# Kernel tuning notes

Measured on AMD Instinct MI355X. Metric: run time of the kernel, lower is better.

Reference implementation:

```python
import jax, jax.numpy as jnp
import numpy as np

DIM = 1024
NUM_HEADS = 16
HEAD_DIM = DIM // NUM_HEADS
SCALE = HEAD_DIM ** -0.5


def setup_inputs() -> dict:
    key = jax.random.key(0)
    k1, k2, k3 = jax.random.split(key, 3)
    x = jax.random.normal(k1, (2, 2048, DIM), dtype=jnp.float32)
    # nn.Linear weights: stored as [out, in]; y = x @ W.T
    w_qkv = jax.random.normal(k2, (3 * DIM, DIM), dtype=jnp.float32) * (DIM ** -0.5)
    w_proj = jax.random.normal(k3, (DIM, DIM), dtype=jnp.float32) * (DIM ** -0.5)
    return {"x": x, "w_qkv": w_qkv, "w_proj": w_proj}


def reference(x, w_qkv, w_proj):
    B, L, D = x.shape
    qkv = jnp.einsum("bld,ed->ble", x, w_qkv)  # [B, L, 3*D]
    qkv = qkv.reshape(B, L, 3, NUM_HEADS, HEAD_DIM).transpose(2, 0, 3, 1, 4)
    q, k, v = qkv[0], qkv[1], qkv[2]  # each [B, H, L, hd]
    attn = jnp.einsum("bhqd,bhkd->bhqk", q, k) * SCALE
    attn = jax.nn.softmax(attn, axis=-1)
    out = jnp.einsum("bhqk,bhkd->bhqd", attn, v)  # [B, H, L, hd]
    out = out.transpose(0, 2, 1, 3).reshape(B, L, D)
    return jnp.einsum("bld,ed->ble", out, w_proj)
```

## Files before the change

kernel.cpp:

```cpp
#include <hip/hip_runtime.h>
#include <math.h>
#include <stdint.h>

#define B_ 2
#define L_ 2048
#define D_ 1024
#define H_ 16
#define HD_ 64
#define QSCALE_ 0.1803368801f

typedef __attribute__((ext_vector_type(8))) short short8;
typedef __attribute__((ext_vector_type(4))) short short4v;
typedef __attribute__((ext_vector_type(4))) float float4v;

#if defined(__has_builtin)
#if __has_builtin(__builtin_amdgcn_exp2f)
#define EXP2F(x) __builtin_amdgcn_exp2f(x)
#endif
#endif
#ifndef EXP2F
#define EXP2F(x) exp2f(x)
#endif

__device__ __forceinline__ short f2bf(float f) {
    union { float f; unsigned u; } x; x.f = f;
    unsigned r = x.u + 0x7fffu + ((x.u >> 16) & 1u);
    return (short)(r >> 16);
}

__device__ __forceinline__ unsigned fbits(float f) {
    union { float f; unsigned u; } x; x.f = f;
    return x.u;
}

__device__ __forceinline__ unsigned pk_bf_trunc(float a, float b) {
    return __builtin_amdgcn_perm(fbits(b), fbits(a), 0x07060302u);
}

__global__ __launch_bounds__(256) void cvt_all(const float* __restrict__ x,
                                               const float* __restrict__ wqkv,
                                               const float* __restrict__ wproj,
                                               short* __restrict__ xb,
                                               short* __restrict__ wqkvb,
                                               short* __restrict__ wprojb) {
    int i = blockIdx.x * 256 + threadIdx.x;
    const float* in;
    short* out;
    int idx;
    if (i < 1048576)      { in = x;     out = xb;     idx = i; }
    else if (i < 1835008) { in = wqkv;  out = wqkvb;  idx = i - 1048576; }
    else                  { in = wproj; out = wprojb; idx = i - 1835008; }
    float4 v = ((const float4*)in)[idx];
    short4v o;
    o.x = f2bf(v.x); o.y = f2bf(v.y); o.z = f2bf(v.z); o.w = f2bf(v.w);
    ((short4v*)out)[idx] = o;
}

__global__ __launch_bounds__(256) void gemm_qkv_bf16(const short* __restrict__ A,
                                                     const short* __restrict__ Bm,
                                                     short* __restrict__ Qb,
                                                     short* __restrict__ Kb,
                                                     short* __restrict__ Vb) {
    __shared__ short smem[16384];
    const int tid = threadIdx.x;
    const int w = tid >> 6, l = tid & 63;
    const int lm = l & 15, q = l >> 4;
    const int bid = blockIdx.x;
    const int xcd = bid & 7;
    const int grp = bid >> 3;
    const int n_tile = xcd + 8 * (grp % 3);
    const int m_tile = grp / 3;
    const int m0 = m_tile * 128, n0 = n_tile * 128;
    const int wm = w >> 1, wn = w & 1;

    const int srow = tid >> 2;
    const int sc8  = (tid & 3) * 8;
    const int soff0 = srow * 32 + sc8;
    const int soff1 = soff0 + 64 * 32;
    const short* Ag = A  + (size_t)(m0 + srow) * 1024 + sc8;
    const short* Bg = Bm + (size_t)(n0 + srow) * 1024 + sc8;

    float4v acc[4][4];
#pragma unroll
    for (int mt = 0; mt < 4; ++mt)
#pragma unroll
        for (int nt = 0; nt < 4; ++nt) acc[mt][nt] = (float4v){0.f, 0.f, 0.f, 0.f};

    {
        short8 a0 = *(const short8*)(Ag);
        short8 a1 = *(const short8*)(Ag + 64 * 1024);
        short8 b0 = *(const short8*)(Bg);
        short8 b1 = *(const short8*)(Bg + 64 * 1024);
        *(short8*)(smem + soff0) = a0;
        *(short8*)(smem + soff1) = a1;
        *(short8*)(smem + 8192 + soff0) = b0;
        *(short8*)(smem + 8192 + soff1) = b1;
    }
    short8 ar0 = *(const short8*)(Ag + 32);
    short8 ar1 = *(const short8*)(Ag + 64 * 1024 + 32);
    short8 br0 = *(const short8*)(Bg + 32);
    short8 br1 = *(const short8*)(Bg + 64 * 1024 + 32);

    for (int t = 0; t < 32; ++t) {
        const int cur = t & 1;
        short* Asc = smem + cur * 4096;
        short* Asn = smem + (1 - cur) * 4096;
        short* Bsc = smem + 8192 + cur * 4096;
        short* Bsn = smem + 8192 + (1 - cur) * 4096;

        __syncthreads();

        if (t < 31) {
            *(short8*)(Asn + soff0) = ar0;
            *(short8*)(Asn + soff1) = ar1;
            *(short8*)(Bsn + soff0) = br0;
            *(short8*)(Bsn + soff1) = br1;
        }
        if (t < 30) {
            const int k0 = (t + 2) * 32;
            ar0 = *(const short8*)(Ag + k0);
            ar1 = *(const short8*)(Ag + 64 * 1024 + k0);
            br0 = *(const short8*)(Bg + k0);
            br1 = *(const short8*)(Bg + 64 * 1024 + k0);
        }

        short8 af[4], bfr[4];
#pragma unroll
        for (int mt = 0; mt < 4; ++mt)
            af[mt] = *(const short8*)(Asc + (wm * 64 + mt * 16 + lm) * 32 + q * 8);
#pragma unroll
        for (int nt = 0; nt < 4; ++nt)
            bfr[nt] = *(const short8*)(Bsc + (wn * 64 + nt * 16 + lm) * 32 + q * 8);
#pragma unroll
        for (int mt = 0; mt < 4; ++mt)
#pragma unroll
            for (int nt = 0; nt < 4; ++nt)
                acc[mt][nt] = __builtin_amdgcn_mfma_f32_16x16x32_bf16(af[mt], bfr[nt], acc[mt][nt], 0, 0, 0);
    }

    const int which = n0 >> 10;
    if (which < 2) {
        short* dst = (which == 0) ? Qb : Kb;
        const float sc = (which == 0) ? QSCALE_ : 1.0f;
#pragma unroll
        for (int half = 0; half < 2; ++half) {
            __syncthreads();
            if (wm == half) {
#pragma unroll
                for (int mt = 0; mt < 4; ++mt)
#pragma unroll
                    for (int nt = 0; nt < 4; ++nt)
#pragma unroll
                        for (int r = 0; r < 4; ++r)
                            smem[(mt * 16 + q * 4 + r) * 128 + wn * 64 + nt * 16 + lm] =
                                f2bf(acc[mt][nt][r] * sc);
            }
            __syncthreads();
#pragma unroll
            for (int j = 0; j < 4; ++j) {
                const int x = tid + 256 * j;
                const int row = x >> 4, c = x & 15;
                short8 v = *(const short8*)(smem + row * 128 + c * 8);
                const int m = m0 + half * 64 + row;
                const int b = m >> 11, ll = m & 2047;
                const int n = n0 + c * 8;
                const int hh = (n & 1023) >> 6, d = n & 63;
                *(short8*)(dst + (((size_t)b * H_ + hh) * L_ + ll) * HD_ + d) = v;
            }
        }
    } else {
        const int mbase = m0 + wm * 64;
        const int b = mbase >> 11;
        const int llb = (mbase & 2047);
#pragma unroll
        for (int mt = 0; mt < 4; ++mt) {
            const int ll = llb + (mt >> 1) * 32 + q * 8 + (mt & 1) * 4;
#pragma unroll
            for (int nt = 0; nt < 4; ++nt) {
                const int n = n0 + wn * 64 + nt * 16 + lm;
                const int h = (n & 1023) >> 6, d = n & 63;
                short4v pk;
                pk.x = f2bf(acc[mt][nt][0]); pk.y = f2bf(acc[mt][nt][1]);
                pk.z = f2bf(acc[mt][nt][2]); pk.w = f2bf(acc[mt][nt][3]);
                *(short4v*)(Vb + (((size_t)b * H_ + h) * HD_ + d) * L_ + ll) = pk;
            }
        }
    }
}

__global__ __launch_bounds__(512) void attn_mfma(const short* __restrict__ Qb,
                                                 const short* __restrict__ Kb,
                                                 const short* __restrict__ Vtg,
                                                 short* __restrict__ Ob) {
    __shared__ short KV[4 * 4096];

    const int tid = threadIdx.x;
    const int w = tid >> 6, l = tid & 63;
    const int lm = l & 15, q = l >> 4;
    const int bid = blockIdx.x;
    const int grp = bid >> 3;
    const int bh = (bid & 7) * 4 + (grp & 3);
    const int qt = grp >> 2;

    const short* Qg = Qb  + ((size_t)bh * L_ + qt * 128) * HD_;
    const short* Kg = Kb  + (size_t)bh * L_ * HD_;
    const short* Vg = Vtg + (size_t)bh * HD_ * L_;

    short* Qs = KV + 8192;
#pragma unroll
    for (int t = 0; t < 2; ++t) {
        int idx = tid + 512 * t;
        int row = idx >> 3, c = idx & 7;
        short8 v = *(const short8*)(Qg + row * 64 + c * 8);
        *(short8*)(Qs + row * 64 + ((c ^ (row & 7)) * 8)) = v;
    }

    const int srow = tid >> 3;
    const int sc   = tid & 7;
    const int koff = srow * 64 + ((sc ^ (srow & 7)) * 8);

    {
        short8 ka = *(const short8*)(Kg + (size_t)srow * 64 + sc * 8);
        short8 va = *(const short8*)(Vg + (size_t)srow * L_ + sc * 8);
        *(short8*)(KV + koff) = ka;
        *(short8*)(KV + 4096 + koff) = va;
    }
    short8 kra = *(const short8*)(Kg + (size_t)(64 + srow) * 64 + sc * 8);
    short8 vra = *(const short8*)(Vg + (size_t)srow * L_ + 64 + sc * 8);

    __syncthreads();

    short8 qf[2];
#pragma unroll
    for (int kh = 0; kh < 2; ++kh) {
        int row = w * 16 + lm;
        int ch = kh * 4 + q;
        qf[kh] = *(const short8*)(Qs + row * 64 + ((ch ^ (row & 7)) * 8));
    }

    int offA0[4], offA1[4], offV[2][4];
#pragma unroll
    for (int nt = 0; nt < 4; ++nt) {
        const int arow = nt * 16 + lm;
        offA0[nt] = arow * 64 + ((q ^ (arow & 7)) * 8);
        offA1[nt] = arow * 64 + (((4 + q) ^ (arow & 7)) * 8);
#pragma unroll
        for (int kh = 0; kh < 2; ++kh)
            offV[kh][nt] = arow * 64 + (((kh * 4 + q) ^ (arow & 7)) * 8);
    }

    float4v o[4];
#pragma unroll
    for (int mt = 0; mt < 4; ++mt) o[mt] = (float4v){0.f, 0.f, 0.f, 0.f};
    float lsum = 0.f;

#pragma unroll 2
    for (int t = 0; t < 32; ++t) {
        const int cur = t & 1;
        short* Kl = KV + cur * 8192;
        short* Vt = Kl + 4096;
        short* Kn = KV + (1 - cur) * 8192;
        short* Vn = Kn + 4096;

        __syncthreads();

        if (t < 31) {
            *(short8*)(Kn + koff) = kra;
            *(short8*)(Vn + koff) = vra;
        }
        if (t < 30) {
            kra = *(const short8*)(Kg + (size_t)((t + 2) * 64 + srow) * 64 + sc * 8);
            vra = *(const short8*)(Vg + (size_t)srow * L_ + (t + 2) * 64 + sc * 8);
        }

        float4v st[4];
#pragma unroll
        for (int nt = 0; nt < 4; ++nt) {
            short8 a0 = *(const short8*)(Kl + offA0[nt]);
            short8 a1 = *(const short8*)(Kl + offA1[nt]);
            float4v z = (float4v){0.f, 0.f, 0.f, 0.f};
            z = __builtin_amdgcn_mfma_f32_16x16x32_bf16(a0, qf[0], z, 0, 0, 0);
            z = __builtin_amdgcn_mfma_f32_16x16x32_bf16(a1, qf[1], z, 0, 0, 0);
            st[nt] = z;
        }

        float e[4][4];
#pragma unroll
        for (int nt = 0; nt < 4; ++nt) {
            e[nt][0] = EXP2F(st[nt][0]);
            e[nt][1] = EXP2F(st[nt][1]);
            e[nt][2] = EXP2F(st[nt][2]);
            e[nt][3] = EXP2F(st[nt][3]);
            lsum += (e[nt][0] + e[nt][1]) + (e[nt][2] + e[nt][3]);
        }
        short8 pb[2];
        {
            union { short8 s8; unsigned u[4]; } p0, p1;
            p0.u[0] = pk_bf_trunc(e[0][0], e[0][1]);
            p0.u[1] = pk_bf_trunc(e[0][2], e[0][3]);
            p0.u[2] = pk_bf_trunc(e[1][0], e[1][1]);
            p0.u[3] = pk_bf_trunc(e[1][2], e[1][3]);
            p1.u[0] = pk_bf_trunc(e[2][0], e[2][1]);
            p1.u[1] = pk_bf_trunc(e[2][2], e[2][3]);
            p1.u[2] = pk_bf_trunc(e[3][0], e[3][1]);
            p1.u[3] = pk_bf_trunc(e[3][2], e[3][3]);
            pb[0] = p0.s8;
            pb[1] = p1.s8;
        }

#pragma unroll
        for (int kh = 0; kh < 2; ++kh)
#pragma unroll
            for (int mt = 0; mt < 4; ++mt) {
                short8 va = *(const short8*)(Vt + offV[kh][mt]);
                o[mt] = __builtin_amdgcn_mfma_f32_16x16x32_bf16(va, pb[kh], o[mt], 0, 0, 0);
            }
    }

    float s = lsum;
    s += __shfl_xor(s, 16);
    s += __shfl_xor(s, 32);
    const float inv = 1.f / s;
    short* OgBase = Ob + ((size_t)bh * L_ + qt * 128) * HD_;
    const int qrow = w * 16 + lm;
#pragma unroll
    for (int mt = 0; mt < 4; ++mt) {
        short4v pk;
        pk.x = f2bf(o[mt][0] * inv);
        pk.y = f2bf(o[mt][1] * inv);
        pk.z = f2bf(o[mt][2] * inv);
        pk.w = f2bf(o[mt][3] * inv);
        *(short4v*)(OgBase + (size_t)qrow * 64 + mt * 16 + q * 4) = pk;
    }
}

__global__ __launch_bounds__(256) void gemm_proj_bf16(const short* __restrict__ Ob,
                                                      const short* __restrict__ Wp,
                                                      float* __restrict__ out) {
    __shared__ short As[2 * 2048];
    __shared__ short Bs[2 * 4096];
    const int tid = threadIdx.x;
    const int w = tid >> 6, l = tid & 63;
    const int lm = l & 15, q = l >> 4;
    const int bid = blockIdx.x;
    const int m0 = (bid >> 3) * 64, n0 = (bid & 7) * 128;
    const int wm = w & 1, wn = w >> 1;
    const int b = m0 >> 11, l0 = m0 & 2047;

    const int srow = tid >> 2;
    const int sc8  = (tid & 3) * 8;
    const int aoff = srow * 32 + sc8;
    const int boff0 = aoff;
    const int boff1 = aoff + 64 * 32;
    const short* Agb = Ob + (((size_t)b * H_) * L_ + l0 + srow) * HD_;
    const short* Bg  = Wp + (size_t)(n0 + srow) * 1024 + sc8;

    float4v acc[2][4];
#pragma unroll
    for (int mt = 0; mt < 2; ++mt)
#pragma unroll
        for (int nt = 0; nt < 4; ++nt) acc[mt][nt] = (float4v){0.f, 0.f, 0.f, 0.f};

    {
        short8 a0 = *(const short8*)(Agb + sc8);
        short8 b0 = *(const short8*)(Bg);
        short8 b1 = *(const short8*)(Bg + 64 * 1024);
        *(short8*)(As + aoff) = a0;
        *(short8*)(Bs + boff0) = b0;
        *(short8*)(Bs + boff1) = b1;
    }
    short8 arx = *(const short8*)(Agb + 32 + sc8);
    short8 brx0 = *(const short8*)(Bg + 32);
    short8 brx1 = *(const short8*)(Bg + 64 * 1024 + 32);

    for (int t = 0; t < 32; ++t) {
        const int cur = t & 1;
        short* Asc = As + cur * 2048;
        short* Asn = As + (1 - cur) * 2048;
        short* Bsc = Bs + cur * 4096;
        short* Bsn = Bs + (1 - cur) * 4096;

        __syncthreads();

        if (t < 31) {
            *(short8*)(Asn + aoff) = arx;
            *(short8*)(Bsn + boff0) = brx0;
            *(short8*)(Bsn + boff1) = brx1;
        }
        if (t < 30) {
            const int tn = t + 2;
            const int hh = tn >> 1, d = (tn & 1) * 32 + sc8;
            arx  = *(const short8*)(Agb + (size_t)hh * L_ * HD_ + d);
            brx0 = *(const short8*)(Bg + tn * 32);
            brx1 = *(const short8*)(Bg + 64 * 1024 + tn * 32);
        }

        short8 af[2], bfr[4];
#pragma unroll
        for (int mt = 0; mt < 2; ++mt)
            af[mt] = *(const short8*)(Asc + (wm * 32 + mt * 16 + lm) * 32 + q * 8);
#pragma unroll
        for (int nt = 0; nt < 4; ++nt)
            bfr[nt] = *(const short8*)(Bsc + (wn * 64 + nt * 16 + lm) * 32 + q * 8);
#pragma unroll
        for (int mt = 0; mt < 2; ++mt)
#pragma unroll
            for (int nt = 0; nt < 4; ++nt)
                acc[mt][nt] = __builtin_amdgcn_mfma_f32_16x16x32_bf16(af[mt], bfr[nt], acc[mt][nt], 0, 0, 0);
    }

#pragma unroll
    for (int mt = 0; mt < 2; ++mt)
#pragma unroll
        for (int nt = 0; nt < 4; ++nt)
#pragma unroll
            for (int r = 0; r < 4; ++r) {
                const int m = m0 + wm * 32 + mt * 16 + q * 4 + r;
                const int n = n0 + wn * 64 + nt * 16 + lm;
                out[(size_t)m * 1024 + n] = acc[mt][nt][r];
            }
}

extern "C" void kernel_launch(void* const* d_in, const int* in_sizes, int n_in,
                              void* d_out, int out_size, void* d_ws, size_t ws_size,
                              hipStream_t stream) {
    (void)in_sizes; (void)n_in; (void)out_size; (void)ws_size;
    const float* x      = (const float*)d_in[0];
    const float* w_qkv  = (const float*)d_in[1];
    const float* w_proj = (const float*)d_in[2];

    char* ws = (char*)d_ws;
    short* xb     = (short*)(ws);
    short* wqkvb  = (short*)(ws + (8u  << 20));
    short* wprojb = (short*)(ws + (14u << 20));
    short* Qb     = (short*)(ws + (16u << 20));
    short* Kb     = (short*)(ws + (24u << 20));
    short* Vb     = (short*)(ws + (32u << 20));
    short* Ob     = (short*)(ws + (40u << 20));

    cvt_all<<<8192, 256, 0, stream>>>(x, w_qkv, w_proj, xb, wqkvb, wprojb);
    gemm_qkv_bf16 <<<768, 256, 0, stream>>>(xb, wqkvb, Qb, Kb, Vb);
    attn_mfma     <<<512, 512, 0, stream>>>(Qb, Kb, Vb, Ob);
    gemm_proj_bf16<<<512, 256, 0, stream>>>(Ob, wprojb, (float*)d_out);
}
```

Before: 174.4 us.

## Pad LDS tiles to stride 40 and use 8 waves in QKV GEMM

Pads the shared-memory row stride of both GEMMs from 32 to 40 bf16 elements so that MFMA fragment reads hit fewer LDS bank conflicts. The QKV GEMM also moves from 256 to 512 threads per block with a 2x4 wave layout, which halves the per-wave accumulator tile and the per-thread staging loads to raise latency hiding. The costs are more LDS per block, more barrier participants, and lower per-wave data reuse.

After: 181.3 us. 4.0% more time.

```diff
diff --git a/kernel.cpp b/kernel.cpp
--- a/kernel.cpp
+++ b/kernel.cpp
@@ -56,12 +56,13 @@
     ((short4v*)out)[idx] = o;
 }
 
-__global__ __launch_bounds__(256) void gemm_qkv_bf16(const short* __restrict__ A,
+#define LDA_ 40
+__global__ __launch_bounds__(512) void gemm_qkv_bf16(const short* __restrict__ A,
                                                      const short* __restrict__ Bm,
                                                      short* __restrict__ Qb,
                                                      short* __restrict__ Kb,
                                                      short* __restrict__ Vb) {
-    __shared__ short smem[16384];
+    __shared__ short smem[20480];
     const int tid = threadIdx.x;
     const int w = tid >> 6, l = tid & 63;
     const int lm = l & 15, q = l >> 4;
@@ -71,70 +72,59 @@
     const int n_tile = xcd + 8 * (grp % 3);
     const int m_tile = grp / 3;
     const int m0 = m_tile * 128, n0 = n_tile * 128;
-    const int wm = w >> 1, wn = w & 1;
+    const int wm = w >> 2, wn = w & 3;
 
     const int srow = tid >> 2;
     const int sc8  = (tid & 3) * 8;
-    const int soff0 = srow * 32 + sc8;
-    const int soff1 = soff0 + 64 * 32;
+    const int soff = srow * LDA_ + sc8;
     const short* Ag = A  + (size_t)(m0 + srow) * 1024 + sc8;
     const short* Bg = Bm + (size_t)(n0 + srow) * 1024 + sc8;
 
-    float4v acc[4][4];
+    float4v acc[4][2];
 #pragma unroll
     for (int mt = 0; mt < 4; ++mt)
 #pragma unroll
-        for (int nt = 0; nt < 4; ++nt) acc[mt][nt] = (float4v){0.f, 0.f, 0.f, 0.f};
+        for (int nt = 0; nt < 2; ++nt) acc[mt][nt] = (float4v){0.f, 0.f, 0.f, 0.f};
 
     {
         short8 a0 = *(const short8*)(Ag);
-        short8 a1 = *(const short8*)(Ag + 64 * 1024);
         short8 b0 = *(const short8*)(Bg);
-        short8 b1 = *(const short8*)(Bg + 64 * 1024);
-        *(short8*)(smem + soff0) = a0;
-        *(short8*)(smem + soff1) = a1;
-        *(short8*)(smem + 8192 + soff0) = b0;
-        *(short8*)(smem + 8192 + soff1) = b1;
-    }
-    short8 ar0 = *(const short8*)(Ag + 32);
-    short8 ar1 = *(const short8*)(Ag + 64 * 1024 + 32);
-    short8 br0 = *(const short8*)(Bg + 32);
-    short8 br1 = *(const short8*)(Bg + 64 * 1024 + 32);
+        *(short8*)(smem + soff) = a0;
+        *(short8*)(smem + 10240 + soff) = b0;
+    }
+    short8 ar = *(const short8*)(Ag + 32);
+    short8 br = *(const short8*)(Bg + 32);
 
     for (int t = 0; t < 32; ++t) {
         const int cur = t & 1;
-        short* Asc = smem + cur * 4096;
-        short* Asn = smem + (1 - cur) * 4096;
-        short* Bsc = smem + 8192 + cur * 4096;
-        short* Bsn = smem + 8192 + (1 - cur) * 4096;
+        short* Asc = smem + cur * 5120;
+        short* Asn = smem + (1 - cur) * 5120;
+        short* Bsc = smem + 10240 + cur * 5120;
+        short* Bsn = smem + 10240 + (1 - cur) * 5120;
 
         __syncthreads();
 
         if (t < 31) {
-            *(short8*)(Asn + soff0) = ar0;
-            *(short8*)(Asn + soff1) = ar1;
-            *(short8*)(Bsn + soff0) = br0;
-            *(short8*)(Bsn + soff1) = br1;
+            *(short8*)(Asn + soff) = ar;
+            *(short8*)(Bsn + soff) = br;
         }
         if (t < 30) {
             const int k0 = (t + 2) * 32;
-            ar0 = *(const short8*)(Ag + k0);
-            ar1 = *(const short8*)(Ag + 64 * 1024 + k0);
-            br0 = *(const short8*)(Bg + k0);
-            br1 = *(const short8*)(Bg + 64 * 1024 + k0);
-        }
-
-        short8 af[4], bfr[4];
+            ar = *(const short8*)(Ag + k0);
+            br = *(const short8*)(Bg + k0);
+        }
+
+        short8 af[4], bfr[2];
 #pragma unroll
         for (int mt = 0; mt < 4; ++mt)
-            af[mt] = *(const short8*)(Asc + (wm * 64 + mt * 16 + lm) * 32 + q * 8);
-#pragma unroll
-        for (int nt = 0; nt < 4; ++nt)
-            bfr[nt] = *(const short8*)(Bsc + (wn * 64 + nt * 16 + lm) * 32 + q * 8);
+            af[mt] = *(const short8*)(Asc + (wm * 64 + mt * 16 + lm) * LDA_ + q * 8);
+#pragma unroll
+        for (int nt = 0; nt < 2; ++nt)
+            bfr[nt] = *(const short8*)(Bsc + (wn * 32 + nt * 16 + lm) * LDA_ + q * 8);
 #pragma unroll
         for (int mt = 0; mt < 4; ++mt)
 #pragma unroll
-            for (int nt = 0; nt < 4; ++nt)
+            for (int nt = 0; nt < 2; ++nt)
                 acc[mt][nt] = __builtin_amdgcn_mfma_f32_16x16x32_bf16(af[mt], bfr[nt], acc[mt][nt], 0, 0, 0);
     }
 
@@ -149,16 +139,16 @@
 #pragma unroll
                 for (int mt = 0; mt < 4; ++mt)
 #pragma unroll
-                    for (int nt = 0; nt < 4; ++nt)
+                    for (int nt = 0; nt < 2; ++nt)
 #pragma unroll
                         for (int r = 0; r < 4; ++r)
-                            smem[(mt * 16 + q * 4 + r) * 128 + wn * 64 + nt * 16 + lm] =
+                            smem[(mt * 16 + q * 4 + r) * 128 + wn * 32 + nt * 16 + lm] =
                                 f2bf(acc[mt][nt][r] * sc);
             }
             __syncthreads();
 #pragma unroll
-            for (int j = 0; j < 4; ++j) {
-                const int x = tid + 256 * j;
+            for (int j = 0; j < 2; ++j) {
+                const int x = tid + 512 * j;
                 const int row = x >> 4, c = x & 15;
                 short8 v = *(const short8*)(smem + row * 128 + c * 8);
                 const int m = m0 + half * 64 + row;
@@ -176,8 +166,8 @@
         for (int mt = 0; mt < 4; ++mt) {
             const int ll = llb + (mt >> 1) * 32 + q * 8 + (mt & 1) * 4;
 #pragma unroll
-            for (int nt = 0; nt < 4; ++nt) {
-                const int n = n0 + wn * 64 + nt * 16 + lm;
+            for (int nt = 0; nt < 2; ++nt) {
+                const int n = n0 + wn * 32 + nt * 16 + lm;
                 const int h = (n & 1023) >> 6, d = n & 63;
                 short4v pk;
                 pk.x = f2bf(acc[mt][nt][0]); pk.y = f2bf(acc[mt][nt][1]);
@@ -337,8 +327,8 @@
 __global__ __launch_bounds__(256) void gemm_proj_bf16(const short* __restrict__ Ob,
                                                       const short* __restrict__ Wp,
                                                       float* __restrict__ out) {
-    __shared__ short As[2 * 2048];
-    __shared__ short Bs[2 * 4096];
+    __shared__ short As[2 * 2560];
+    __shared__ short Bs[2 * 5120];
     const int tid = threadIdx.x;
     const int w = tid >> 6, l = tid & 63;
     const int lm = l & 15, q = l >> 4;
@@ -349,9 +339,9 @@
 
     const int srow = tid >> 2;
     const int sc8  = (tid & 3) * 8;
-    const int aoff = srow * 32 + sc8;
+    const int aoff = srow * LDA_ + sc8;
     const int boff0 = aoff;
-    const int boff1 = aoff + 64 * 32;
+    const int boff1 = aoff + 64 * LDA_;
     const short* Agb = Ob + (((size_t)b * H_) * L_ + l0 + srow) * HD_;
     const short* Bg  = Wp + (size_t)(n0 + srow) * 1024 + sc8;
 
@@ -375,10 +365,10 @@
 
     for (int t = 0; t < 32; ++t) {
         const int cur = t & 1;
-        short* Asc = As + cur * 2048;
-        short* Asn = As + (1 - cur) * 2048;
-        short* Bsc = Bs + cur * 4096;
-        short* Bsn = Bs + (1 - cur) * 4096;
+        short* Asc = As + cur * 2560;
+        short* Asn = As + (1 - cur) * 2560;
+        short* Bsc = Bs + cur * 5120;
+        short* Bsn = Bs + (1 - cur) * 5120;
 
         __syncthreads();
 
@@ -398,10 +388,10 @@
         short8 af[2], bfr[4];
 #pragma unroll
         for (int mt = 0; mt < 2; ++mt)
-            af[mt] = *(const short8*)(Asc + (wm * 32 + mt * 16 + lm) * 32 + q * 8);
+            af[mt] = *(const short8*)(Asc + (wm * 32 + mt * 16 + lm) * LDA_ + q * 8);
 #pragma unroll
         for (int nt = 0; nt < 4; ++nt)
-            bfr[nt] = *(const short8*)(Bsc + (wn * 64 + nt * 16 + lm) * 32 + q * 8);
+            bfr[nt] = *(const short8*)(Bsc + (wn * 64 + nt * 16 + lm) * LDA_ + q * 8);
 #pragma unroll
         for (int mt = 0; mt < 2; ++mt)
 #pragma unroll
@@ -439,7 +429,7 @@
     short* Ob     = (short*)(ws + (40u << 20));
 
     cvt_all<<<8192, 256, 0, stream>>>(x, w_qkv, w_proj, xb, wqkvb, wprojb);
-    gemm_qkv_bf16 <<<768, 256, 0, stream>>>(xb, wqkvb, Qb, Kb, Vb);
+    gemm_qkv_bf16 <<<768, 512, 0, stream>>>(xb, wqkvb, Qb, Kb, Vb);
     attn_mfma     <<<512, 512, 0, stream>>>(Qb, Kb, Vb, Ob);
     gemm_proj_bf16<<<512, 256, 0, stream>>>(Ob, wprojb, (float*)d_out);
 }
```
